# Performance work log

Hardware: AMD Instinct MI355X
Metric: run time of the kernel (lower is better)

## Reference

```python
import jax, jax.numpy as jnp
import numpy as np

NUM_CLASSES = 8
NUM_MAPS = 4
FEAT_C = 2048  # ResNet-50 layer4 channels
HW = 14        # spatial size (448/32)


def setup_inputs() -> dict:
    key = jax.random.key(0)
    k1, k2, k3, k4, k5 = jax.random.split(key, 5)
    B = 64
    x = jax.random.normal(k1, (B, FEAT_C, HW, HW), dtype=jnp.float32)
    down_w = jax.random.normal(k2, (NUM_CLASSES * NUM_MAPS, FEAT_C), dtype=jnp.float32) * 0.02
    down_b = jax.random.normal(k3, (NUM_CLASSES * NUM_MAPS,), dtype=jnp.float32) * 0.02
    fc_w = jax.random.normal(k4, (NUM_CLASSES, 2 * FEAT_C), dtype=jnp.float32) * 0.02
    fc_b = jax.random.normal(k5, (NUM_CLASSES,), dtype=jnp.float32) * 0.02
    return {"x": x, "down_w": down_w, "down_b": down_b, "fc_w": fc_w, "fc_b": fc_b}


def reference(x, down_w, down_b, fc_w, fc_b):
    B = x.shape[0]
    x_ori = x  # [B, 2048, 14, 14] (ResNet features output)
    # downconv: 1x1 conv 2048 -> num_classes*num_maps
    xc = jnp.einsum('bchw,oc->bohw', x_ori, down_w) + down_b[None, :, None, None]  # [B,32,14,14]
    # GMP over full 14x14 window -> [B, 32]
    gmp = jnp.max(xc, axis=(2, 3))
    # spatial_pooling = ClassWisePool(num_maps): mean over groups of num_maps channels
    scores = gmp.reshape(B, NUM_CLASSES, NUM_MAPS).mean(axis=2)  # [B, 8]
    x_out = jax.nn.log_softmax(scores, axis=1)  # first output
    # class-wise pool on the full conv map: [B,32,14,14] -> [B,8,14,14]
    xcp = xc.reshape(B, NUM_CLASSES, NUM_MAPS, HW, HW).mean(axis=2)
    # modulate each class map by its (log-softmax) score
    xcp = xcp * x_out[:, :, None, None]
    # spatial_pooling2 = ClassWisePool(num_classes): mean over 8 class channels -> [B,1,14,14]
    sal = xcp.mean(axis=1, keepdims=True)
    prod = sal * x_ori  # [B,2048,14,14] via broadcast (fused, no copies)
    cat = jnp.concatenate([x_ori, prod], axis=1)  # [B,4096,14,14]
    # GAP 14x14 -> [B,4096]
    gap = cat.mean(axis=(2, 3))
    logits2 = gap @ fc_w.T + fc_b  # [B,8]
    x_conv_out = jax.nn.log_softmax(logits2, axis=1)
    return (x_out, x_conv_out)
```

## Files before the change

kernel.cpp:

```cpp
#include <hip/hip_runtime.h>

#define NCH 2048
#define HW 196
#define NB 64
#define NOUT 48
#define NCHUNK 8
#define CPC (NCH / NCHUNK)
#define KS_PER_BLK (CPC / 32)
#define KGTOT (NCH / 32)
#define NT 13
#define MT 3
#define TILE_F (32 * HW)
#define TILE_V4 (TILE_F / 4)
#define SLAB (NT * NOUT * 16)
#define SLAB8 (SLAB / 2)
#define ROWSTRIDE (16 * NOUT)

typedef __attribute__((ext_vector_type(8))) short bf16x8;
typedef __attribute__((ext_vector_type(4))) float f32x4;
typedef __attribute__((ext_vector_type(4))) int i32x4;

__device__ __forceinline__ short f2bf(float f) {
    unsigned int u = __float_as_uint(f);
    u = u + 0x7fffu + ((u >> 16) & 1u);
    return (short)(u >> 16);
}

__device__ __forceinline__ unsigned long long pack2(float a, float b) {
    union { float f[2]; unsigned long long u; } t;
    t.f[0] = a; t.f[1] = b; return t.u;
}

__global__ void build_afrag(const float* __restrict__ down_w,
                            const float* __restrict__ fc_w,
                            bf16x8* __restrict__ afrag,
                            unsigned int* __restrict__ cnt) {
    int t = blockIdx.x * 256 + threadIdx.x;
    if (blockIdx.x == 0 && threadIdx.x < NB) cnt[threadIdx.x] = 0;
    if (t >= KGTOT * MT * 64) return;
    int lane = t & 63;
    int frag = t >> 6;
    int mt = frag % MT;
    int kg = frag / MT;
    int o = mt * 16 + (lane & 15);
    int kq = lane >> 4;
    bf16x8 v;
#pragma unroll
    for (int j = 0; j < 8; ++j) {
        int c = kg * 32 + kq * 2 + (j & 1) + ((j >> 1) << 3);
        float w;
        if (o < 32)      w = down_w[o * NCH + c];
        else if (o < 40) w = fc_w[(o - 32) * (2 * NCH) + NCH + c];
        else             w = fc_w[(o - 40) * (2 * NCH) + c];
        v[j] = f2bf(w);
    }
    afrag[frag * 64 + lane] = v;
}

struct FinSM {
    float Ts[NOUT * HW];
    float red[256];
    float gmp[32];
    float score[8];
    float xo[8];
    float sal[HW];
    float logit[8];
};

__global__ __launch_bounds__(256) void conv_fin(const float* __restrict__ x,
                                                const bf16x8* __restrict__ afrag,
                                                const float* __restrict__ down_b,
                                                const float* __restrict__ fc_b,
                                                float* __restrict__ part,
                                                unsigned int* __restrict__ cnt,
                                                float* __restrict__ out) {
    __shared__ union {
        float ldsx[2][TILE_F];
        FinSM fin;
    } sm;
    __shared__ int lastS;

    const int chunk = blockIdx.x;
    const int b = blockIdx.y;
    const int tid = threadIdx.x;
    const int wave = tid >> 6;
    const int lane = tid & 63;
    const int nsub = lane & 15;
    const int kq = lane >> 4;

    f32x4 acc[4][MT];
#pragma unroll
    for (int i = 0; i < 4; ++i)
#pragma unroll
        for (int m = 0; m < MT; ++m)
            acc[i][m] = (f32x4){0.f, 0.f, 0.f, 0.f};

    int pidx[4];
#pragma unroll
    for (int i = 0; i < 4; ++i) {
        int p = (wave + 4 * i) * 16 + nsub;
        pidx[i] = (p < HW) ? p : (HW - 1);
    }

    const float* xtile0 = x + ((size_t)b * NCH + (size_t)chunk * CPC) * HW;

    auto stage = [&](int ks, int bb) {
        const float* g = xtile0 + (size_t)ks * TILE_F;
#pragma unroll
        for (int r = 0; r < 7; ++r) {
            int q = r * 256 + tid;
            if (q < TILE_V4) {
                __builtin_amdgcn_global_load_lds(
                    (const __attribute__((address_space(1))) unsigned int*)(g + (size_t)q * 4),
                    (__attribute__((address_space(3))) unsigned int*)(&sm.ldsx[bb][(r * 256 + wave * 64) * 4]),
                    16, 0, 0);
            }
        }
    };

    stage(0, 0);

    for (int ks = 0; ks < KS_PER_BLK; ++ks) {
        __syncthreads();
        if (ks + 1 < KS_PER_BLK) stage(ks + 1, (ks + 1) & 1);

        const int kg = chunk * KS_PER_BLK + ks;
        bf16x8 a0 = afrag[(kg * MT + 0) * 64 + lane];
        bf16x8 a1 = afrag[(kg * MT + 1) * 64 + lane];
        bf16x8 a2 = afrag[(kg * MT + 2) * 64 + lane];

        const float* base = &sm.ldsx[ks & 1][kq * 2 * HW];
#pragma unroll
        for (int i = 0; i < 4; ++i) {
            const float* bp = base + pidx[i];
            unsigned int u[8];
#pragma unroll
            for (int j = 0; j < 8; ++j)
                u[j] = __float_as_uint(bp[((j & 1) + ((j >> 1) << 3)) * HW]) + 0x8000u;
            i32x4 bi;
            bi[0] = (int)__builtin_amdgcn_perm(u[1], u[0], 0x07060302u);
            bi[1] = (int)__builtin_amdgcn_perm(u[3], u[2], 0x07060302u);
            bi[2] = (int)__builtin_amdgcn_perm(u[5], u[4], 0x07060302u);
            bi[3] = (int)__builtin_amdgcn_perm(u[7], u[6], 0x07060302u);
            bf16x8 bv = __builtin_bit_cast(bf16x8, bi);
            acc[i][0] = __builtin_amdgcn_mfma_f32_16x16x32_bf16(a0, bv, acc[i][0], 0, 0, 0);
            acc[i][1] = __builtin_amdgcn_mfma_f32_16x16x32_bf16(a1, bv, acc[i][1], 0, 0, 0);
            acc[i][2] = __builtin_amdgcn_mfma_f32_16x16x32_bf16(a2, bv, acc[i][2], 0, 0, 0);
        }
    }

    float* pb = part + (size_t)(b * NCHUNK + chunk) * SLAB;
#pragma unroll
    for (int i = 0; i < 4; ++i) {
        int nt = wave + 4 * i;
        if (nt < NT) {
            float* d = pb + nt * ROWSTRIDE + nsub * NOUT + kq * 4;
#pragma unroll
            for (int m = 0; m < MT; ++m) {
                unsigned long long lo = pack2(acc[i][m][0], acc[i][m][1]);
                unsigned long long hi = pack2(acc[i][m][2], acc[i][m][3]);
                unsigned long long* q = (unsigned long long*)(d + m * 16);
                __hip_atomic_store(q,     lo, __ATOMIC_RELAXED, __HIP_MEMORY_SCOPE_AGENT);
                __hip_atomic_store(q + 1, hi, __ATOMIC_RELAXED, __HIP_MEMORY_SCOPE_AGENT);
            }
        }
    }

    __syncthreads();
    if (tid == 0) {
        unsigned int old = __hip_atomic_fetch_add(&cnt[b], 1u,
                                                  __ATOMIC_RELAXED, __HIP_MEMORY_SCOPE_AGENT);
        int last = (old == NCHUNK - 1);
        if (last)
            (void)__hip_atomic_load(&cnt[b], __ATOMIC_ACQUIRE, __HIP_MEMORY_SCOPE_AGENT);
        lastS = last;
    }
    __syncthreads();
    if (!lastS) return;

    {
        const unsigned long long* basep =
            (const unsigned long long*)(part + (size_t)b * NCHUNK * SLAB);
        for (int i8 = tid; i8 < SLAB8; i8 += 256) {
            float sx = 0.f, sy = 0.f;
#pragma unroll
            for (int ch = 0; ch < NCHUNK; ++ch) {
                unsigned long long u = __hip_atomic_load(
                    basep + (size_t)ch * SLAB8 + i8,
                    __ATOMIC_RELAXED, __HIP_MEMORY_SCOPE_AGENT);
                union { unsigned long long u; float f[2]; } t;
                t.u = u;
                sx += t.f[0]; sy += t.f[1];
            }
            int idx = i8 * 2;
            int ntv = idx / ROWSTRIDE;
            int rem = idx - ntv * ROWSTRIDE;
            int ns = rem / NOUT;
            int o0 = rem - ns * NOUT;
            int p = ntv * 16 + ns;
            if (p < HW) {
                sm.fin.Ts[o0 * HW + p] = sx;
                sm.fin.Ts[(o0 + 1) * HW + p] = sy;
            }
        }
    }
    __syncthreads();

    {
        int o = tid >> 3, s8 = tid & 7;
        float m = -1e30f;
        for (int p = s8; p < HW; p += 8) m = fmaxf(m, sm.fin.Ts[o * HW + p]);
        sm.fin.red[tid] = m;
    }
    __syncthreads();
    if (tid < 32) {
        float m = sm.fin.red[tid * 8];
#pragma unroll
        for (int j = 1; j < 8; ++j) m = fmaxf(m, sm.fin.red[tid * 8 + j]);
        sm.fin.gmp[tid] = m + down_b[tid];
    }
    __syncthreads();

    if (tid < 8)
        sm.fin.score[tid] = 0.25f * (sm.fin.gmp[4 * tid] + sm.fin.gmp[4 * tid + 1] +
                                     sm.fin.gmp[4 * tid + 2] + sm.fin.gmp[4 * tid + 3]);
    __syncthreads();

    if (tid < 8) {
        float m = -1e30f;
        for (int k = 0; k < 8; ++k) m = fmaxf(m, sm.fin.score[k]);
        float se = 0.f;
        for (int k = 0; k < 8; ++k) se += expf(sm.fin.score[k] - m);
        float xo = sm.fin.score[tid] - m - logf(se);
        sm.fin.xo[tid] = xo;
        out[b * 8 + tid] = xo;
    }
    __syncthreads();

    if (tid < HW) {
        float s = 0.f;
#pragma unroll
        for (int k = 0; k < 8; ++k) {
            float bs = down_b[4 * k] + down_b[4 * k + 1] +
                       down_b[4 * k + 2] + down_b[4 * k + 3];
            float rs = sm.fin.Ts[(4 * k) * HW + tid] + sm.fin.Ts[(4 * k + 1) * HW + tid] +
                       sm.fin.Ts[(4 * k + 2) * HW + tid] + sm.fin.Ts[(4 * k + 3) * HW + tid] + bs;
            s += sm.fin.xo[k] * rs;
        }
        sm.fin.sal[tid] = s * (1.f / 32.f);
    }
    __syncthreads();

    {
        int c = tid >> 5, s32 = tid & 31;
        float t = 0.f;
        for (int p = s32; p < HW; p += 32)
            t += sm.fin.Ts[(40 + c) * HW + p] + sm.fin.sal[p] * sm.fin.Ts[(32 + c) * HW + p];
        sm.fin.red[tid] = t;
    }
    __syncthreads();
    if (tid < 8) {
        float t = 0.f;
#pragma unroll
        for (int j = 0; j < 32; ++j) t += sm.fin.red[tid * 32 + j];
        sm.fin.logit[tid] = t * (1.f / 196.f) + fc_b[tid];
    }
    __syncthreads();

    if (tid < 8) {
        float m = -1e30f;
        for (int k = 0; k < 8; ++k) m = fmaxf(m, sm.fin.logit[k]);
        float se = 0.f;
        for (int k = 0; k < 8; ++k) se += expf(sm.fin.logit[k] - m);
        out[NB * 8 + b * 8 + tid] = sm.fin.logit[tid] - m - logf(se);
    }
}

extern "C" void kernel_launch(void* const* d_in, const int* in_sizes, int n_in,
                              void* d_out, int out_size, void* d_ws, size_t ws_size,
                              hipStream_t stream) {
    const float* x      = (const float*)d_in[0];
    const float* down_w = (const float*)d_in[1];
    const float* down_b = (const float*)d_in[2];
    const float* fc_w   = (const float*)d_in[3];
    const float* fc_b   = (const float*)d_in[4];
    float* out = (float*)d_out;

    bf16x8* afrag = (bf16x8*)d_ws;
    float* part = (float*)((char*)d_ws + (size_t)KGTOT * MT * 64 * 16);
    unsigned int* cnt = (unsigned int*)((char*)part + (size_t)NB * NCHUNK * SLAB * 4);

    build_afrag<<<(KGTOT * MT * 64 + 255) / 256, 256, 0, stream>>>(down_w, fc_w, afrag, cnt);
    conv_fin<<<dim3(NCHUNK, NB), 256, 0, stream>>>(x, afrag, down_b, fc_b, part, cnt, out);
}
```

Baseline: 190.0 us.

## Double channel split and reduce partial sums with float atomics instead of slabs

Result: slower. 291.2 us (+53.3%).

```diff
diff --git a/kernel.cpp b/kernel.cpp
--- a/kernel.cpp
+++ b/kernel.cpp
@@ -4,7 +4,7 @@
 #define HW 196
 #define NB 64
 #define NOUT 48
-#define NCHUNK 8
+#define NCHUNK 16
 #define CPC (NCH / NCHUNK)
 #define KS_PER_BLK (CPC / 32)
 #define KGTOT (NCH / 32)
@@ -26,17 +26,18 @@
     return (short)(u >> 16);
 }
 
-__device__ __forceinline__ unsigned long long pack2(float a, float b) {
-    union { float f[2]; unsigned long long u; } t;
-    t.f[0] = a; t.f[1] = b; return t.u;
-}
-
 __global__ void build_afrag(const float* __restrict__ down_w,
                             const float* __restrict__ fc_w,
                             bf16x8* __restrict__ afrag,
+                            float* __restrict__ accb,
                             unsigned int* __restrict__ cnt) {
     int t = blockIdx.x * 256 + threadIdx.x;
     if (blockIdx.x == 0 && threadIdx.x < NB) cnt[threadIdx.x] = 0;
+    {
+        float4* az = (float4*)accb;
+        for (int i = t; i < NB * SLAB / 4; i += 12288)
+            az[i] = (float4){0.f, 0.f, 0.f, 0.f};
+    }
     if (t >= KGTOT * MT * 64) return;
     int lane = t & 63;
     int frag = t >> 6;
@@ -71,7 +72,7 @@
                                                 const bf16x8* __restrict__ afrag,
                                                 const float* __restrict__ down_b,
                                                 const float* __restrict__ fc_b,
-                                                float* __restrict__ part,
+                                                float* __restrict__ accb,
                                                 unsigned int* __restrict__ cnt,
                                                 float* __restrict__ out) {
     __shared__ union {
@@ -149,20 +150,17 @@
         }
     }
 
-    float* pb = part + (size_t)(b * NCHUNK + chunk) * SLAB;
+    float* ab = accb + (size_t)b * SLAB;
 #pragma unroll
     for (int i = 0; i < 4; ++i) {
         int nt = wave + 4 * i;
         if (nt < NT) {
-            float* d = pb + nt * ROWSTRIDE + nsub * NOUT + kq * 4;
-#pragma unroll
-            for (int m = 0; m < MT; ++m) {
-                unsigned long long lo = pack2(acc[i][m][0], acc[i][m][1]);
-                unsigned long long hi = pack2(acc[i][m][2], acc[i][m][3]);
-                unsigned long long* q = (unsigned long long*)(d + m * 16);
-                __hip_atomic_store(q,     lo, __ATOMIC_RELAXED, __HIP_MEMORY_SCOPE_AGENT);
-                __hip_atomic_store(q + 1, hi, __ATOMIC_RELAXED, __HIP_MEMORY_SCOPE_AGENT);
-            }
+            float* d = ab + nt * ROWSTRIDE + nsub * NOUT + kq * 4;
+#pragma unroll
+            for (int m = 0; m < MT; ++m)
+#pragma unroll
+                for (int r = 0; r < 4; ++r)
+                    unsafeAtomicAdd(&d[m * 16 + r], acc[i][m][r]);
         }
     }
 
@@ -180,18 +178,12 @@
 
     {
         const unsigned long long* basep =
-            (const unsigned long long*)(part + (size_t)b * NCHUNK * SLAB);
+            (const unsigned long long*)(accb + (size_t)b * SLAB);
         for (int i8 = tid; i8 < SLAB8; i8 += 256) {
-            float sx = 0.f, sy = 0.f;
-#pragma unroll
-            for (int ch = 0; ch < NCHUNK; ++ch) {
-                unsigned long long u = __hip_atomic_load(
-                    basep + (size_t)ch * SLAB8 + i8,
-                    __ATOMIC_RELAXED, __HIP_MEMORY_SCOPE_AGENT);
-                union { unsigned long long u; float f[2]; } t;
-                t.u = u;
-                sx += t.f[0]; sy += t.f[1];
-            }
+            unsigned long long u = __hip_atomic_load(
+                basep + i8, __ATOMIC_RELAXED, __HIP_MEMORY_SCOPE_AGENT);
+            union { unsigned long long u; float f[2]; } t;
+            t.u = u;
             int idx = i8 * 2;
             int ntv = idx / ROWSTRIDE;
             int rem = idx - ntv * ROWSTRIDE;
@@ -199,8 +191,8 @@
             int o0 = rem - ns * NOUT;
             int p = ntv * 16 + ns;
             if (p < HW) {
-                sm.fin.Ts[o0 * HW + p] = sx;
-                sm.fin.Ts[(o0 + 1) * HW + p] = sy;
+                sm.fin.Ts[o0 * HW + p] = t.f[0];
+                sm.fin.Ts[(o0 + 1) * HW + p] = t.f[1];
             }
         }
     }
@@ -287,9 +279,9 @@
     float* out = (float*)d_out;
 
     bf16x8* afrag = (bf16x8*)d_ws;
-    float* part = (float*)((char*)d_ws + (size_t)KGTOT * MT * 64 * 16);
-    unsigned int* cnt = (unsigned int*)((char*)part + (size_t)NB * NCHUNK * SLAB * 4);
-
-    build_afrag<<<(KGTOT * MT * 64 + 255) / 256, 256, 0, stream>>>(down_w, fc_w, afrag, cnt);
-    conv_fin<<<dim3(NCHUNK, NB), 256, 0, stream>>>(x, afrag, down_b, fc_b, part, cnt, out);
-}
+    float* accb = (float*)((char*)d_ws + (size_t)KGTOT * MT * 64 * 16);
+    unsigned int* cnt = (unsigned int*)((char*)accb + (size_t)NB * SLAB * 4);
+
+    build_afrag<<<(KGTOT * MT * 64 + 255) / 256, 256, 0, stream>>>(down_w, fc_w, afrag, accb, cnt);
+    conv_fin<<<dim3(NCHUNK, NB), 256, 0, stream>>>(x, afrag, down_b, fc_b, accb, cnt, out);
+}
```
